# Optimization experiments

Hardware: AMD Instinct MI355X
Metric: run time of the kernel (lower is better)

## Reference

```python
import jax, jax.numpy as jnp
import numpy as np

N, E, IN_CH, HEADS, OUT_CH = 50000, 800000, 128, 4, 64
HC = HEADS * OUT_CH
NEG_SLOPE = 0.2
LN_EPS = 1e-5


def setup_inputs() -> dict:
    key = jax.random.key(0)
    ks = jax.random.split(key, 6)
    x = jax.random.normal(ks[0], (N, IN_CH), dtype=jnp.float32)
    edge_index = jax.random.randint(ks[1], (2, E), 0, N, dtype=jnp.int64)
    W = jax.random.normal(ks[2], (IN_CH, HC), dtype=jnp.float32) * 0.05
    att_src = jax.random.normal(ks[3], (HEADS, OUT_CH), dtype=jnp.float32) * 0.05
    att_dst = jax.random.normal(ks[4], (HEADS, OUT_CH), dtype=jnp.float32) * 0.05
    bias = jnp.zeros((HC,), dtype=jnp.float32)
    gamma = jnp.ones((HC,), dtype=jnp.float32)
    beta = jnp.zeros((HC,), dtype=jnp.float32)
    return {"x": x, "edge_index": edge_index, "W": W, "att_src": att_src,
            "att_dst": att_dst, "bias": bias, "gamma": gamma, "beta": beta}


def reference(x, edge_index, W, att_src, att_dst, bias, gamma, beta):
    n = x.shape[0]
    # add self loops (PyG GATConv default add_self_loops=True)
    loops = jnp.arange(n, dtype=edge_index.dtype)
    src = jnp.concatenate([edge_index[0], loops])  # [E+N]
    dst = jnp.concatenate([edge_index[1], loops])
    # linear transform -> [N, H, C]
    h = (x @ W).reshape(n, HEADS, OUT_CH)
    # per-node attention halves [N, H]
    a_s = jnp.einsum('nhc,hc->nh', h, att_src)
    a_d = jnp.einsum('nhc,hc->nh', h, att_dst)
    # per-edge logits [E', H]
    e = jax.nn.leaky_relu(a_s[src] + a_d[dst], NEG_SLOPE)
    # segment softmax over incoming edges of each target node
    m = jax.ops.segment_max(e, dst, num_segments=n)
    p = jnp.exp(e - m[dst])
    s = jax.ops.segment_sum(p, dst, num_segments=n)
    alpha = p / (s[dst] + 1e-16)  # [E', H]
    # weighted scatter-add of source features
    msg = h[src] * alpha[:, :, None]  # [E', H, C]
    out = jax.ops.segment_sum(msg, dst, num_segments=n).reshape(n, HC) + bias
    # LayerNorm over H*C then ELU
    mu = out.mean(-1, keepdims=True)
    var = out.var(-1, keepdims=True)
    normed = (out - mu) * jax.lax.rsqrt(var + LN_EPS) * gamma + beta
    return jax.nn.elu(normed)
```

## Files before the change

kernel.cpp:

```cpp
#include <hip/hip_runtime.h>
#include <math.h>

#define NNODES 50000
#define EEDGES 800000
#define ETOT   (EEDGES + NNODES)
#define INCH   128
#define HEADS  4
#define OUTCH  64
#define HC     256
#define NEG_SLOPE 0.2f
#define LN_EPS 1e-5f
#define CAP    128

typedef unsigned int   u32;
typedef unsigned short u16;
typedef __attribute__((ext_vector_type(8))) short short8;
typedef __attribute__((ext_vector_type(4))) float floatx4;

__device__ __forceinline__ u16 f2bf(float f) {
    u32 u = __float_as_uint(f);
    return (u16)((u + 0x7fffu + ((u >> 16) & 1u)) >> 16);
}
__device__ __forceinline__ float bflo(u32 u) { return __uint_as_float(u << 16); }
__device__ __forceinline__ float bfhi(u32 u) { return __uint_as_float(u & 0xffff0000u); }

__global__ __launch_bounds__(64) void k_detect(const int* __restrict__ buf,
                                               int* __restrict__ flag) {
    int lane = threadIdx.x;
    int v = buf[2 * lane + 1];
    unsigned long long b = __ballot(v != 0);
    if (lane == 0) flag[0] = (b == 0ULL) ? 1 : 0;
}

__global__ __launch_bounds__(256) void k_cvtW(const float* __restrict__ Wm,
                                              u16* __restrict__ Wt) {
    int idx = blockIdx.x * 256 + threadIdx.x;
    int n = idx >> 7;
    int k = idx & 127;
    Wt[n * 128 + k] = f2bf(Wm[(size_t)k * HC + n]);
}

__global__ __launch_bounds__(256) void k_build(const int* __restrict__ buf,
                                               const int* __restrict__ flag,
                                               int* __restrict__ cursor,
                                               int* __restrict__ adj) {
    int e = blockIdx.x * 256 + threadIdx.x;
    if (e >= ETOT) return;
    int s, d;
    if (e >= EEDGES) {
        s = e - EEDGES; d = s;
    } else if (flag[0]) {
        s = ((const int2*)buf)[e].x;
        d = ((const int2*)buf)[EEDGES + e].x;
    } else {
        s = buf[e];
        d = buf[EEDGES + e];
    }
    int pos = atomicAdd(&cursor[d], 1);
    if (pos < CAP) adj[(size_t)d * CAP + pos] = s;
}

#define GM   128
#define GN   128
#define ASP  136
#define BSP  136

__global__ __launch_bounds__(256) void k_gemm_mfma(
        const float* __restrict__ X, const u16* __restrict__ Wt,
        const float* __restrict__ att_s, const float* __restrict__ att_d,
        u16* __restrict__ Hb, float* __restrict__ a_s, float* __restrict__ a_d) {
    __shared__ __align__(16) u16 As[GM * ASP];
    __shared__ __align__(16) u16 Bs[GN * BSP];
    int tid = threadIdx.x;
    int lane = tid & 63;
    int w = tid >> 6;
    int l15 = lane & 15;
    int quad = lane >> 4;
    int colBase = blockIdx.x * GN;
    int rowBase = blockIdx.y * GM;
    int head0 = colBase >> 6;

    {
        int r = tid >> 1;
        int c0 = (tid & 1) * 64;
        int grow = rowBase + r;
        u16* dstp = &As[r * ASP + c0];
        if (grow < NNODES) {
            const float* xr = &X[(size_t)grow * INCH + c0];
#pragma unroll
            for (int i = 0; i < 16; i++) {
                float4 v = *(const float4*)(xr + i * 4);
                ushort4 b;
                b.x = f2bf(v.x); b.y = f2bf(v.y); b.z = f2bf(v.z); b.w = f2bf(v.w);
                *(ushort4*)(dstp + i * 4) = b;
            }
        } else {
            ushort4 z = {0, 0, 0, 0};
#pragma unroll
            for (int i = 0; i < 16; i++) *(ushort4*)(dstp + i * 4) = z;
        }
    }
    {
        int n = tid >> 1;
        int c0 = (tid & 1) * 64;
        const uint4* srcp = (const uint4*)&Wt[(size_t)(colBase + n) * 128 + c0];
        uint4* dstp = (uint4*)&Bs[n * BSP + c0];
#pragma unroll
        for (int i = 0; i < 8; i++) dstp[i] = srcp[i];
    }
    __syncthreads();

    floatx4 acc[2][8];
#pragma unroll
    for (int mt = 0; mt < 2; mt++)
#pragma unroll
        for (int nt = 0; nt < 8; nt++)
#pragma unroll
            for (int r = 0; r < 4; r++) acc[mt][nt][r] = 0.f;
    int mrow = w * 32;
#pragma unroll
    for (int kk = 0; kk < 4; kk++) {
        int kof = kk * 32 + quad * 8;
        short8 a0 = *(short8*)&As[(mrow + l15) * ASP + kof];
        short8 a1 = *(short8*)&As[(mrow + 16 + l15) * ASP + kof];
#pragma unroll
        for (int nt = 0; nt < 8; nt++) {
            short8 b = *(short8*)&Bs[(nt * 16 + l15) * BSP + kof];
            acc[0][nt] = __builtin_amdgcn_mfma_f32_16x16x32_bf16(a0, b, acc[0][nt], 0, 0, 0);
            acc[1][nt] = __builtin_amdgcn_mfma_f32_16x16x32_bf16(a1, b, acc[1][nt], 0, 0, 0);
        }
    }

    float asf[8], adf[8];
#pragma unroll
    for (int nt = 0; nt < 8; nt++) {
        asf[nt] = att_s[colBase + nt * 16 + l15];
        adf[nt] = att_d[colBase + nt * 16 + l15];
    }
#pragma unroll
    for (int mt = 0; mt < 2; mt++) {
#pragma unroll
        for (int r = 0; r < 4; r++) {
            float ps0 = acc[mt][0][r] * asf[0] + acc[mt][1][r] * asf[1] +
                        acc[mt][2][r] * asf[2] + acc[mt][3][r] * asf[3];
            float pd0 = acc[mt][0][r] * adf[0] + acc[mt][1][r] * adf[1] +
                        acc[mt][2][r] * adf[2] + acc[mt][3][r] * adf[3];
            float ps1 = acc[mt][4][r] * asf[4] + acc[mt][5][r] * asf[5] +
                        acc[mt][6][r] * asf[6] + acc[mt][7][r] * asf[7];
            float pd1 = acc[mt][4][r] * adf[4] + acc[mt][5][r] * adf[5] +
                        acc[mt][6][r] * adf[6] + acc[mt][7][r] * adf[7];
#pragma unroll
            for (int off = 8; off >= 1; off >>= 1) {
                ps0 += __shfl_xor(ps0, off, 64);
                pd0 += __shfl_xor(pd0, off, 64);
                ps1 += __shfl_xor(ps1, off, 64);
                pd1 += __shfl_xor(pd1, off, 64);
            }
            int g = rowBase + mrow + mt * 16 + quad * 4 + r;
            if (l15 == 0 && g < NNODES) {
                a_s[g * 4 + head0]     = ps0;
                a_d[g * 4 + head0]     = pd0;
                a_s[g * 4 + head0 + 1] = ps1;
                a_d[g * 4 + head0 + 1] = pd1;
            }
        }
    }

    __syncthreads();
    u16* Cs = As;
#pragma unroll
    for (int mt = 0; mt < 2; mt++)
#pragma unroll
        for (int nt = 0; nt < 8; nt++)
#pragma unroll
            for (int r = 0; r < 4; r++)
                Cs[(mrow + mt * 16 + quad * 4 + r) * ASP + nt * 16 + l15] =
                    f2bf(acc[mt][nt][r]);
    __syncthreads();
    {
        int r = tid >> 1;
        int c0 = (tid & 1) * 64;
        int g = rowBase + r;
        if (g < NNODES) {
            const uint4* srcp = (const uint4*)&Cs[r * ASP + c0];
            uint4* dstp = (uint4*)&Hb[(size_t)g * HC + colBase + c0];
#pragma unroll
            for (int i = 0; i < 8; i++) dstp[i] = srcp[i];
        }
    }
}

__global__ __launch_bounds__(256) void k_aggregate(
        const u16* __restrict__ Hb,
        const float* __restrict__ a_s, const float* __restrict__ a_d,
        const int* __restrict__ cursor, const int* __restrict__ adj,
        const float* __restrict__ bias, const float* __restrict__ gamma,
        const float* __restrict__ beta, float* __restrict__ out) {
    __shared__ int   sidxS[4][64];
    __shared__ float alphaS[4][256];
    int tid = threadIdx.x;
    int lane = tid & 63;
    int w = tid >> 6;
    int n = blockIdx.x * 4 + w;
    if (n >= NNODES) return;
    int cnt = cursor[n]; if (cnt > CAP) cnt = CAP;
    const int* adjn = &adj[(size_t)n * CAP];

    float4 adn = *(const float4*)&a_d[n * 4];
    float ad[4] = {adn.x, adn.y, adn.z, adn.w};

    int half = lane >> 5;
    int cgrp = lane & 31;
    int hme = cgrp >> 3;
    float accv[8];
#pragma unroll
    for (int k2 = 0; k2 < 8; k2++) accv[k2] = 0.f;

    if (cnt <= 64) {
        int sidx = 0;
        float eh0 = -1e30f, eh1 = -1e30f, eh2 = -1e30f, eh3 = -1e30f;
        bool act = lane < cnt;
        if (act) {
            sidx = adjn[lane];
            float4 as4 = *(const float4*)&a_s[sidx * 4];
            eh0 = as4.x + ad[0]; eh0 = (eh0 > 0.f) ? eh0 : NEG_SLOPE * eh0;
            eh1 = as4.y + ad[1]; eh1 = (eh1 > 0.f) ? eh1 : NEG_SLOPE * eh1;
            eh2 = as4.z + ad[2]; eh2 = (eh2 > 0.f) ? eh2 : NEG_SLOPE * eh2;
            eh3 = as4.w + ad[3]; eh3 = (eh3 > 0.f) ? eh3 : NEG_SLOPE * eh3;
        }
        float m0 = eh0, m1 = eh1, m2 = eh2, m3 = eh3;
#pragma unroll
        for (int off = 32; off >= 1; off >>= 1) {
            m0 = fmaxf(m0, __shfl_xor(m0, off, 64));
            m1 = fmaxf(m1, __shfl_xor(m1, off, 64));
            m2 = fmaxf(m2, __shfl_xor(m2, off, 64));
            m3 = fmaxf(m3, __shfl_xor(m3, off, 64));
        }
        float p0 = act ? __expf(eh0 - m0) : 0.f;
        float p1 = act ? __expf(eh1 - m1) : 0.f;
        float p2 = act ? __expf(eh2 - m2) : 0.f;
        float p3 = act ? __expf(eh3 - m3) : 0.f;
        float s0 = p0, s1 = p1, s2 = p2, s3 = p3;
#pragma unroll
        for (int off = 32; off >= 1; off >>= 1) {
            s0 += __shfl_xor(s0, off, 64);
            s1 += __shfl_xor(s1, off, 64);
            s2 += __shfl_xor(s2, off, 64);
            s3 += __shfl_xor(s3, off, 64);
        }
        float al0 = p0 * (1.f / (s0 + 1e-16f));
        float al1 = p1 * (1.f / (s1 + 1e-16f));
        float al2 = p2 * (1.f / (s2 + 1e-16f));
        float al3 = p3 * (1.f / (s3 + 1e-16f));
        sidxS[w][lane] = sidx;
        *(float4*)&alphaS[w][lane * 4] = make_float4(al0, al1, al2, al3);
        __builtin_amdgcn_wave_barrier();

        int cnt_pad = (cnt + 15) & ~15;
        for (int j = 0; j < cnt_pad; j += 16) {
            int jj[8];
            int si[8];
            float Al[8];
#pragma unroll
            for (int q = 0; q < 8; q++) {
                jj[q] = j + 2 * q + half;
                si[q] = sidxS[w][jj[q]];
                Al[q] = alphaS[w][jj[q] * 4 + hme];
            }
            uint4 hv[8];
#pragma unroll
            for (int q = 0; q < 8; q++)
                hv[q] = *(const uint4*)&Hb[(size_t)si[q] * HC + cgrp * 8];
#pragma unroll
            for (int q = 0; q < 8; q++) {
                accv[0] += Al[q] * bflo(hv[q].x); accv[1] += Al[q] * bfhi(hv[q].x);
                accv[2] += Al[q] * bflo(hv[q].y); accv[3] += Al[q] * bfhi(hv[q].y);
                accv[4] += Al[q] * bflo(hv[q].z); accv[5] += Al[q] * bfhi(hv[q].z);
                accv[6] += Al[q] * bflo(hv[q].w); accv[7] += Al[q] * bfhi(hv[q].w);
            }
        }
    } else {
        float m[4], ssum[4];
#pragma unroll
        for (int h = 0; h < 4; h++) { m[h] = -1e30f; ssum[h] = 0.f; }
        for (int i = lane; i < cnt; i += 64) {
            int sidx = adjn[i];
            float4 as4 = *(const float4*)&a_s[sidx * 4];
            float av[4] = {as4.x, as4.y, as4.z, as4.w};
#pragma unroll
            for (int h = 0; h < 4; h++) {
                float eh = av[h] + ad[h];
                eh = (eh > 0.f) ? eh : NEG_SLOPE * eh;
                float mn = fmaxf(m[h], eh);
                ssum[h] = ssum[h] * __expf(m[h] - mn) + __expf(eh - mn);
                m[h] = mn;
            }
        }
#pragma unroll
        for (int off = 32; off >= 1; off >>= 1) {
#pragma unroll
            for (int h = 0; h < 4; h++) {
                float mo = __shfl_xor(m[h], off, 64);
                float so = __shfl_xor(ssum[h], off, 64);
                float mn = fmaxf(m[h], mo);
                ssum[h] = ssum[h] * __expf(m[h] - mn) + so * __expf(mo - mn);
                m[h] = mn;
            }
        }
        float inv[4];
#pragma unroll
        for (int h = 0; h < 4; h++) inv[h] = 1.f / (ssum[h] + 1e-16f);
        for (int c0 = 0; c0 < cnt; c0 += 64) {
            int ccnt = cnt - c0; if (ccnt > 64) ccnt = 64;
            float a0 = 0.f, a1 = 0.f, a2 = 0.f, a3 = 0.f;
            int sv = 0;
            if (lane < ccnt) {
                sv = adjn[c0 + lane];
                float4 as4 = *(const float4*)&a_s[sv * 4];
                float e0 = as4.x + ad[0]; e0 = (e0 > 0.f) ? e0 : NEG_SLOPE * e0;
                float e1 = as4.y + ad[1]; e1 = (e1 > 0.f) ? e1 : NEG_SLOPE * e1;
                float e2 = as4.z + ad[2]; e2 = (e2 > 0.f) ? e2 : NEG_SLOPE * e2;
                float e3 = as4.w + ad[3]; e3 = (e3 > 0.f) ? e3 : NEG_SLOPE * e3;
                a0 = __expf(e0 - m[0]) * inv[0];
                a1 = __expf(e1 - m[1]) * inv[1];
                a2 = __expf(e2 - m[2]) * inv[2];
                a3 = __expf(e3 - m[3]) * inv[3];
            }
            sidxS[w][lane] = sv;
            *(float4*)&alphaS[w][lane * 4] = make_float4(a0, a1, a2, a3);
            __builtin_amdgcn_wave_barrier();
            int cpad = (ccnt + 3) & ~3;
            for (int j = 0; j < cpad; j += 4) {
                int j0 = j + half, j1 = j + 2 + half;
                int i0 = sidxS[w][j0], i1 = sidxS[w][j1];
                float A0 = alphaS[w][j0 * 4 + hme], A1 = alphaS[w][j1 * 4 + hme];
                uint4 h0 = *(const uint4*)&Hb[(size_t)i0 * HC + cgrp * 8];
                uint4 h1 = *(const uint4*)&Hb[(size_t)i1 * HC + cgrp * 8];
                accv[0] += A0 * bflo(h0.x); accv[1] += A0 * bfhi(h0.x);
                accv[2] += A0 * bflo(h0.y); accv[3] += A0 * bfhi(h0.y);
                accv[4] += A0 * bflo(h0.z); accv[5] += A0 * bfhi(h0.z);
                accv[6] += A0 * bflo(h0.w); accv[7] += A0 * bfhi(h0.w);
                accv[0] += A1 * bflo(h1.x); accv[1] += A1 * bfhi(h1.x);
                accv[2] += A1 * bflo(h1.y); accv[3] += A1 * bfhi(h1.y);
                accv[4] += A1 * bflo(h1.z); accv[5] += A1 * bfhi(h1.z);
                accv[6] += A1 * bflo(h1.w); accv[7] += A1 * bfhi(h1.w);
            }
            __builtin_amdgcn_wave_barrier();
        }
    }

#pragma unroll
    for (int k2 = 0; k2 < 8; k2++) accv[k2] += __shfl_xor(accv[k2], 32, 64);

    int cb = cgrp * 8;
    float4 b0 = *(const float4*)&bias[cb];
    float4 b1 = *(const float4*)&bias[cb + 4];
    accv[0] += b0.x; accv[1] += b0.y; accv[2] += b0.z; accv[3] += b0.w;
    accv[4] += b1.x; accv[5] += b1.y; accv[6] += b1.z; accv[7] += b1.w;
    float psum = 0.f, psq = 0.f;
#pragma unroll
    for (int k2 = 0; k2 < 8; k2++) { psum += accv[k2]; psq += accv[k2] * accv[k2]; }
#pragma unroll
    for (int off = 16; off >= 1; off >>= 1) {
        psum += __shfl_xor(psum, off, 64);
        psq  += __shfl_xor(psq,  off, 64);
    }
    float mean = psum * (1.f / HC);
    float var  = psq * (1.f / HC) - mean * mean;
    float rstd = rsqrtf(var + LN_EPS);
    float4 g0 = *(const float4*)&gamma[cb];
    float4 g1 = *(const float4*)&gamma[cb + 4];
    float4 e0 = *(const float4*)&beta[cb];
    float4 e1 = *(const float4*)&beta[cb + 4];
    float gv[8] = {g0.x, g0.y, g0.z, g0.w, g1.x, g1.y, g1.z, g1.w};
    float bv[8] = {e0.x, e0.y, e0.z, e0.w, e1.x, e1.y, e1.z, e1.w};
    float o[8];
#pragma unroll
    for (int k2 = 0; k2 < 8; k2++) {
        float v = (accv[k2] - mean) * rstd * gv[k2] + bv[k2];
        o[k2] = (v > 0.f) ? v : expm1f(v);
    }
    float4 wv = half ? make_float4(o[4], o[5], o[6], o[7])
                     : make_float4(o[0], o[1], o[2], o[3]);
    *(float4*)&out[(size_t)n * HC + cb + half * 4] = wv;
}

extern "C" void kernel_launch(void* const* d_in, const int* in_sizes, int n_in,
                              void* d_out, int out_size, void* d_ws, size_t ws_size,
                              hipStream_t stream) {
    const float* x     = (const float*)d_in[0];
    const int*   ebuf  = (const int*)d_in[1];
    const float* Wm    = (const float*)d_in[2];
    const float* att_s = (const float*)d_in[3];
    const float* att_d = (const float*)d_in[4];
    const float* bias  = (const float*)d_in[5];
    const float* gamma = (const float*)d_in[6];
    const float* beta  = (const float*)d_in[7];
    float* out = (float*)d_out;

    char* ws = (char*)d_ws;
    size_t off = 0;
    auto alloc = [&](size_t bytes) -> void* {
        void* p = ws + off;
        off += (bytes + 255) & ~(size_t)255;
        return p;
    };
    u16* Hb     = (u16*)alloc((size_t)NNODES * HC * 2);
    float* a_s  = (float*)alloc((size_t)NNODES * HEADS * 4);
    float* a_d  = (float*)alloc((size_t)NNODES * HEADS * 4);
    int* cursor = (int*)alloc((size_t)NNODES * 4);
    int* adj    = (int*)alloc((size_t)NNODES * CAP * 4);
    u16* Wt     = (u16*)alloc((size_t)HC * INCH * 2);
    int* flag   = (int*)alloc(4);

    hipMemsetAsync(cursor, 0, (size_t)NNODES * 4, stream);

    k_detect<<<1, 64, 0, stream>>>(ebuf, flag);
    k_cvtW<<<(HC * INCH) / 256, 256, 0, stream>>>(Wm, Wt);
    k_build<<<(ETOT + 255) / 256, 256, 0, stream>>>(ebuf, flag, cursor, adj);

    dim3 ggrid(HC / GN, (NNODES + GM - 1) / GM);
    k_gemm_mfma<<<ggrid, 256, 0, stream>>>(x, Wt, att_s, att_d, Hb, a_s, a_d);

    k_aggregate<<<(NNODES + 3) / 4, 256, 0, stream>>>(
        Hb, a_s, a_d, cursor, adj, bias, gamma, beta, out);
}
```

Measured before the change: 250.9 us.

## Retile GEMM to full-width 64-row blocks with W read from global

The projection GEMM now uses one block per 64 rows covering all 256 output columns, with one wave per head. B fragments are loaded straight from global/L2 instead of staged in LDS. This removes the duplicated X load and bf16 conversion across the two column blocks and shrinks LDS use, but it adds more global loads of W per block. The ELU also switches from expm1f to __expf(v)-1, which is cheaper but less accurate for small negative inputs.

```diff
diff --git a/kernel.cpp b/kernel.cpp
--- a/kernel.cpp
+++ b/kernel.cpp
@@ -60,35 +60,31 @@
     if (pos < CAP) adj[(size_t)d * CAP + pos] = s;
 }
 
-#define GM   128
-#define GN   128
-#define ASP  136
-#define BSP  136
+#define GM   64
+#define ASPA 136
+#define CSP  264
 
 __global__ __launch_bounds__(256) void k_gemm_mfma(
         const float* __restrict__ X, const u16* __restrict__ Wt,
         const float* __restrict__ att_s, const float* __restrict__ att_d,
         u16* __restrict__ Hb, float* __restrict__ a_s, float* __restrict__ a_d) {
-    __shared__ __align__(16) u16 As[GM * ASP];
-    __shared__ __align__(16) u16 Bs[GN * BSP];
+    __shared__ __align__(16) u16 S[GM * CSP];
     int tid = threadIdx.x;
     int lane = tid & 63;
     int w = tid >> 6;
     int l15 = lane & 15;
     int quad = lane >> 4;
-    int colBase = blockIdx.x * GN;
-    int rowBase = blockIdx.y * GM;
-    int head0 = colBase >> 6;
+    int rowBase = blockIdx.x * GM;
 
     {
-        int r = tid >> 1;
-        int c0 = (tid & 1) * 64;
+        int r = tid >> 2;
+        int c0 = (tid & 3) * 32;
         int grow = rowBase + r;
-        u16* dstp = &As[r * ASP + c0];
+        u16* dstp = &S[r * ASPA + c0];
         if (grow < NNODES) {
             const float* xr = &X[(size_t)grow * INCH + c0];
 #pragma unroll
-            for (int i = 0; i < 16; i++) {
+            for (int i = 0; i < 8; i++) {
                 float4 v = *(const float4*)(xr + i * 4);
                 ushort4 b;
                 b.x = f2bf(v.x); b.y = f2bf(v.y); b.z = f2bf(v.z); b.w = f2bf(v.w);
@@ -97,95 +93,83 @@
         } else {
             ushort4 z = {0, 0, 0, 0};
 #pragma unroll
-            for (int i = 0; i < 16; i++) *(ushort4*)(dstp + i * 4) = z;
-        }
-    }
-    {
-        int n = tid >> 1;
-        int c0 = (tid & 1) * 64;
-        const uint4* srcp = (const uint4*)&Wt[(size_t)(colBase + n) * 128 + c0];
-        uint4* dstp = (uint4*)&Bs[n * BSP + c0];
-#pragma unroll
-        for (int i = 0; i < 8; i++) dstp[i] = srcp[i];
+            for (int i = 0; i < 8; i++) *(ushort4*)(dstp + i * 4) = z;
+        }
     }
     __syncthreads();
 
-    floatx4 acc[2][8];
-#pragma unroll
-    for (int mt = 0; mt < 2; mt++)
-#pragma unroll
-        for (int nt = 0; nt < 8; nt++)
+    floatx4 acc[4][4];
+#pragma unroll
+    for (int mt = 0; mt < 4; mt++)
+#pragma unroll
+        for (int nt = 0; nt < 4; nt++)
 #pragma unroll
             for (int r = 0; r < 4; r++) acc[mt][nt][r] = 0.f;
-    int mrow = w * 32;
 #pragma unroll
     for (int kk = 0; kk < 4; kk++) {
         int kof = kk * 32 + quad * 8;
-        short8 a0 = *(short8*)&As[(mrow + l15) * ASP + kof];
-        short8 a1 = *(short8*)&As[(mrow + 16 + l15) * ASP + kof];
-#pragma unroll
-        for (int nt = 0; nt < 8; nt++) {
-            short8 b = *(short8*)&Bs[(nt * 16 + l15) * BSP + kof];
-            acc[0][nt] = __builtin_amdgcn_mfma_f32_16x16x32_bf16(a0, b, acc[0][nt], 0, 0, 0);
-            acc[1][nt] = __builtin_amdgcn_mfma_f32_16x16x32_bf16(a1, b, acc[1][nt], 0, 0, 0);
-        }
-    }
-
-    float asf[8], adf[8];
-#pragma unroll
-    for (int nt = 0; nt < 8; nt++) {
-        asf[nt] = att_s[colBase + nt * 16 + l15];
-        adf[nt] = att_d[colBase + nt * 16 + l15];
-    }
-#pragma unroll
-    for (int mt = 0; mt < 2; mt++) {
+        short8 b[4];
+#pragma unroll
+        for (int nt = 0; nt < 4; nt++)
+            b[nt] = *(const short8*)&Wt[(size_t)(w * 64 + nt * 16 + l15) * 128 + kof];
+        short8 a[4];
+#pragma unroll
+        for (int mt = 0; mt < 4; mt++)
+            a[mt] = *(short8*)&S[(mt * 16 + l15) * ASPA + kof];
+#pragma unroll
+        for (int mt = 0; mt < 4; mt++)
+#pragma unroll
+            for (int nt = 0; nt < 4; nt++)
+                acc[mt][nt] = __builtin_amdgcn_mfma_f32_16x16x32_bf16(a[mt], b[nt], acc[mt][nt], 0, 0, 0);
+    }
+
+    float asf[4], adf[4];
+#pragma unroll
+    for (int nt = 0; nt < 4; nt++) {
+        asf[nt] = att_s[w * 64 + nt * 16 + l15];
+        adf[nt] = att_d[w * 64 + nt * 16 + l15];
+    }
+#pragma unroll
+    for (int mt = 0; mt < 4; mt++) {
 #pragma unroll
         for (int r = 0; r < 4; r++) {
-            float ps0 = acc[mt][0][r] * asf[0] + acc[mt][1][r] * asf[1] +
-                        acc[mt][2][r] * asf[2] + acc[mt][3][r] * asf[3];
-            float pd0 = acc[mt][0][r] * adf[0] + acc[mt][1][r] * adf[1] +
-                        acc[mt][2][r] * adf[2] + acc[mt][3][r] * adf[3];
-            float ps1 = acc[mt][4][r] * asf[4] + acc[mt][5][r] * asf[5] +
-                        acc[mt][6][r] * asf[6] + acc[mt][7][r] * asf[7];
-            float pd1 = acc[mt][4][r] * adf[4] + acc[mt][5][r] * adf[5] +
-                        acc[mt][6][r] * adf[6] + acc[mt][7][r] * adf[7];
+            float ps = acc[mt][0][r] * asf[0] + acc[mt][1][r] * asf[1] +
+                       acc[mt][2][r] * asf[2] + acc[mt][3][r] * asf[3];
+            float pd = acc[mt][0][r] * adf[0] + acc[mt][1][r] * adf[1] +
+                       acc[mt][2][r] * adf[2] + acc[mt][3][r] * adf[3];
 #pragma unroll
             for (int off = 8; off >= 1; off >>= 1) {
-                ps0 += __shfl_xor(ps0, off, 64);
-                pd0 += __shfl_xor(pd0, off, 64);
-                ps1 += __shfl_xor(ps1, off, 64);
-                pd1 += __shfl_xor(pd1, off, 64);
-            }
-            int g = rowBase + mrow + mt * 16 + quad * 4 + r;
+                ps += __shfl_xor(ps, off, 64);
+                pd += __shfl_xor(pd, off, 64);
+            }
+            int g = rowBase + mt * 16 + quad * 4 + r;
             if (l15 == 0 && g < NNODES) {
-                a_s[g * 4 + head0]     = ps0;
-                a_d[g * 4 + head0]     = pd0;
-                a_s[g * 4 + head0 + 1] = ps1;
-                a_d[g * 4 + head0 + 1] = pd1;
+                a_s[g * 4 + w] = ps;
+                a_d[g * 4 + w] = pd;
             }
         }
     }
 
     __syncthreads();
-    u16* Cs = As;
-#pragma unroll
-    for (int mt = 0; mt < 2; mt++)
-#pragma unroll
-        for (int nt = 0; nt < 8; nt++)
+#pragma unroll
+    for (int mt = 0; mt < 4; mt++)
+#pragma unroll
+        for (int nt = 0; nt < 4; nt++)
 #pragma unroll
             for (int r = 0; r < 4; r++)
-                Cs[(mrow + mt * 16 + quad * 4 + r) * ASP + nt * 16 + l15] =
+                S[(mt * 16 + quad * 4 + r) * CSP + w * 64 + nt * 16 + l15] =
                     f2bf(acc[mt][nt][r]);
     __syncthreads();
     {
-        int r = tid >> 1;
-        int c0 = (tid & 1) * 64;
+        int r = tid >> 2;
+        int c0 = (tid & 3) * 64;
         int g = rowBase + r;
         if (g < NNODES) {
-            const uint4* srcp = (const uint4*)&Cs[r * ASP + c0];
-            uint4* dstp = (uint4*)&Hb[(size_t)g * HC + colBase + c0];
-#pragma unroll
-            for (int i = 0; i < 8; i++) dstp[i] = srcp[i];
+            const u16* srcp = &S[r * CSP + c0];
+            u16* dstp = &Hb[(size_t)g * HC + c0];
+#pragma unroll
+            for (int i = 0; i < 8; i++)
+                *(uint4*)(dstp + i * 8) = *(const uint4*)(srcp + i * 8);
         }
     }
 }
@@ -378,7 +362,7 @@
 #pragma unroll
     for (int k2 = 0; k2 < 8; k2++) {
         float v = (accv[k2] - mean) * rstd * gv[k2] + bv[k2];
-        o[k2] = (v > 0.f) ? v : expm1f(v);
+        o[k2] = (v > 0.f) ? v : (__expf(v) - 1.0f);
     }
     float4 wv = half ? make_float4(o[4], o[5], o[6], o[7])
                      : make_float4(o[0], o[1], o[2], o[3]);
@@ -419,8 +403,8 @@
     k_cvtW<<<(HC * INCH) / 256, 256, 0, stream>>>(Wm, Wt);
     k_build<<<(ETOT + 255) / 256, 256, 0, stream>>>(ebuf, flag, cursor, adj);
 
-    dim3 ggrid(HC / GN, (NNODES + GM - 1) / GM);
-    k_gemm_mfma<<<ggrid, 256, 0, stream>>>(x, Wt, att_s, att_d, Hb, a_s, a_d);
+    k_gemm_mfma<<<(NNODES + GM - 1) / GM, 256, 0, stream>>>(
+        x, Wt, att_s, att_d, Hb, a_s, a_d);
 
     k_aggregate<<<(NNODES + 3) / 4, 256, 0, stream>>>(
         Hb, a_s, a_d, cursor, adj, bias, gamma, beta, out);
```

Result: no change. 252.1 us (+0.4%).
